# Kernel tuning notes

Measured on AMD Instinct MI355X. Metric: run time of the kernel, lower is better.

The kernel has to match this reference:

```python
import jax, jax.numpy as jnp
import numpy as np

H, D, HID = 16, 128, 2048
B, S = 2, 2048
NUM_BLOCKS, BLOCK_SIZE = 32, 128


def _rope(x, cos, sin):
    # x: [T, H, D]; cos/sin: [T, D/2] (neox / rotate-half style)
    half = x.shape[-1] // 2
    x1, x2 = x[..., :half], x[..., half:]
    c = cos[:, None, :]
    s = sin[:, None, :]
    return jnp.concatenate([x1 * c - x2 * s, x2 * c + x1 * s], axis=-1)


def setup_inputs() -> dict:
    key = jax.random.key(0)
    ks = jax.random.split(key, 6)
    T = B * S
    hidden_states = jax.random.normal(ks[0], (T, HID), jnp.float32)
    wqkv = jax.random.normal(ks[1], (HID, 3 * HID), jnp.float32) * 0.02
    bqkv = jax.random.normal(ks[2], (3 * HID,), jnp.float32) * 0.02
    wo = jax.random.normal(ks[3], (HID, HID), jnp.float32) * 0.02
    # rotary tables, base 10000, dim = head_size
    inv_freq = 1.0 / (10000.0 ** (jnp.arange(0, D, 2, dtype=jnp.float32) / D))  # [D/2]
    pos = jnp.tile(jnp.arange(S, dtype=jnp.float32), B)  # positions per token [T]
    ang = pos[:, None] * inv_freq[None, :]  # [T, D/2]
    cos, sin = jnp.cos(ang), jnp.sin(ang)
    k_cache = jnp.zeros((NUM_BLOCKS, BLOCK_SIZE, H, D), jnp.float32)
    v_cache = jnp.zeros((NUM_BLOCKS, BLOCK_SIZE, H, D), jnp.float32)
    cu_seqlen_prefill = jnp.array([0, S, 2 * S], jnp.int32)
    slots = jnp.arange(T, dtype=jnp.int32)
    return {"hidden_states": hidden_states, "cos": cos, "sin": sin,
            "wqkv": wqkv, "bqkv": bqkv, "wo": wo,
            "k_cache": k_cache, "v_cache": v_cache,
            "cu_seqlen_prefill": cu_seqlen_prefill, "slots": slots, "max_s": S}


def reference(hidden_states, cos, sin, wqkv, bqkv, wo, k_cache, v_cache,
              cu_seqlen_prefill, slots, max_s):
    T = hidden_states.shape[0]
    # fused QKV projection (c_attn)
    qkv = hidden_states @ wqkv + bqkv  # [T, 3*H*D]
    q, k, v = jnp.split(qkv, [H * D, 2 * H * D], axis=1)
    q = q.reshape(T, H, D)
    k = k.reshape(T, H, D)
    v = v.reshape(T, H, D)
    # rotary embedding on q and k (in-place in torch; functional here)
    q = _rope(q, cos, sin)
    k = _rope(k, cos, sin)
    # reshape_and_cache: scatter post-rope k and v into paged KV cache by slot
    kc = k_cache.reshape(-1, H, D).at[slots].set(k).reshape(k_cache.shape)
    vc = v_cache.reshape(-1, H, D).at[slots].set(v).reshape(v_cache.shape)
    # prefill flash attention: varlen causal; equal-length sequences here
    b, s = T // max_s, max_s
    qb = q.reshape(b, s, H, D)
    kb = k.reshape(b, s, H, D)
    vb = v.reshape(b, s, H, D)
    scale = D ** -0.5
    scores = jnp.einsum('bqhd,bkhd->bhqk', qb, kb) * scale  # [B,H,S,S]
    causal = jnp.tril(jnp.ones((s, s), bool))
    scores = jnp.where(causal[None, None], scores, jnp.finfo(scores.dtype).min)
    probs = jax.nn.softmax(scores, axis=-1)
    attn = jnp.einsum('bhqk,bkhd->bqhd', probs, vb).reshape(T, H * D)
    out = attn @ wo  # c_proj, no bias
    return out, kc, vc
```

## Files before the change

### kernel.cpp

```cpp
#include <hip/hip_runtime.h>

using f32x4  = __attribute__((ext_vector_type(4))) float;
using frag16 = __attribute__((ext_vector_type(8))) short;
using s16x4  = __attribute__((ext_vector_type(4))) short;
using s16x8  = __attribute__((ext_vector_type(8))) short;

#define DI __device__ __forceinline__

constexpr int HID  = 2048;
constexpr int NH   = 16;
constexpr int HD   = 128;
constexpr int TT   = 4096;
constexpr int SEQ  = 2048;
constexpr int NQKV = 3 * HID;

DI short f2bf(float f) {
  unsigned u = __builtin_bit_cast(unsigned, f);
  unsigned r = (u + 0x7fffu + ((u >> 16) & 1u)) >> 16;
  return (short)r;
}
DI float bf2f(short s) {
  unsigned u = ((unsigned)(unsigned short)s) << 16;
  return __builtin_bit_cast(float, u);
}

struct alignas(8) S4h { short a, b, c, d; };

__global__ void conv_f32_bf16(const float* __restrict__ in, short* __restrict__ out) {
  int gid = blockIdx.x * 256 + threadIdx.x;
  const float4* in4 = (const float4*)in;
  float4 v = in4[gid];
  S4h o{f2bf(v.x), f2bf(v.y), f2bf(v.z), f2bf(v.w)};
  ((S4h*)out)[gid] = o;
}

template <bool IN_F32>
__global__ void transpose_conv(const void* __restrict__ in_, short* __restrict__ out,
                               int ldin, int R) {
  __shared__ float t[64][65];
  const float* inf = (const float*)in_;
  const short* ins = (const short*)in_;
  int tid = threadIdx.x;
  int bx = blockIdx.x, by = blockIdx.y;
#pragma unroll
  for (int i = 0; i < 16; i++) {
    int idx = i * 256 + tid;
    int r = idx >> 6, c = idx & 63;
    size_t gi = (size_t)(by * 64 + r) * ldin + bx * 64 + c;
    t[r][c] = IN_F32 ? inf[gi] : bf2f(ins[gi]);
  }
  __syncthreads();
#pragma unroll
  for (int i = 0; i < 16; i++) {
    int idx = i * 256 + tid;
    int r = idx >> 6, c = idx & 63;
    out[(size_t)(bx * 64 + r) * R + by * 64 + c] = f2bf(t[c][r]);
  }
}

#define GLDS(src, dst)                                                     \
  __builtin_amdgcn_global_load_lds(                                        \
      (const __attribute__((address_space(1))) void*)(src),                \
      (__attribute__((address_space(3))) void*)(dst), 16, 0, 0)

template <bool ADD_BIAS, bool OUT_BF16>
__global__ __launch_bounds__(256, 2) void gemm_bt(
    const short* __restrict__ A, const short* __restrict__ Bt,
    const float* __restrict__ bias, void* __restrict__ Cout,
    int M, int N, int K) {
  __shared__ alignas(16) short Al[128 * 64];
  __shared__ alignas(16) short Bl[128 * 64];
  const int tid = threadIdx.x;
  const int wid = tid >> 6, lane = tid & 63;
  const int wr = wid >> 1, wc = wid & 1;
  const int l15 = lane & 15, lg = lane >> 4;
  const int row0 = blockIdx.y * 128, col0 = blockIdx.x * 128;
  const int lr8 = lane >> 3, l7 = lane & 7;

  f32x4 acc[4][4];
#pragma unroll
  for (int i = 0; i < 4; i++)
#pragma unroll
    for (int j = 0; j < 4; j++) acc[i][j] = {0.f, 0.f, 0.f, 0.f};

  for (int kt = 0; kt < K; kt += 64) {
#pragma unroll
    for (int c = 0; c < 4; c++) {
      int chunk = c * 4 + wid;
      int r = chunk * 8 + lr8;
      int ke = (l7 * 8) ^ ((r & 7) * 8);
      GLDS(A + (size_t)(row0 + r) * K + kt + ke, Al + chunk * 512);
      GLDS(Bt + (size_t)(col0 + r) * K + kt + ke, Bl + chunk * 512);
    }
    __syncthreads();
#pragma unroll
    for (int kk = 0; kk < 2; kk++) {
      frag16 af[4], bfv[4];
#pragma unroll
      for (int ai = 0; ai < 4; ai++) {
        int r = wr * 64 + ai * 16 + l15;
        int k0 = kk * 32 + lg * 8;
        af[ai] = *(const frag16*)(Al + r * 64 + (k0 ^ ((r & 7) * 8)));
      }
#pragma unroll
      for (int bj = 0; bj < 4; bj++) {
        int r = wc * 64 + bj * 16 + l15;
        int k0 = kk * 32 + lg * 8;
        bfv[bj] = *(const frag16*)(Bl + r * 64 + (k0 ^ ((r & 7) * 8)));
      }
#pragma unroll
      for (int ai = 0; ai < 4; ai++)
#pragma unroll
        for (int bj = 0; bj < 4; bj++)
          acc[ai][bj] = __builtin_amdgcn_mfma_f32_16x16x32_bf16(
              af[ai], bfv[bj], acc[ai][bj], 0, 0, 0);
    }
    __syncthreads();
  }
#pragma unroll
  for (int ai = 0; ai < 4; ai++) {
#pragma unroll
    for (int bj = 0; bj < 4; bj++) {
      int row = row0 + wr * 64 + ai * 16 + lg * 4;
      int col = col0 + wc * 64 + bj * 16 + l15;
      float bv = 0.f;
      if (ADD_BIAS) bv = bias[col];
#pragma unroll
      for (int r = 0; r < 4; r++) {
        float v = acc[ai][bj][r] + bv;
        if (OUT_BF16)
          ((short*)Cout)[(size_t)(row + r) * N + col] = f2bf(v);
        else
          ((float*)Cout)[(size_t)(row + r) * N + col] = v;
      }
    }
  }
}

__global__ void rope_scatter(const short* __restrict__ qkv, const float* __restrict__ cs,
                             const float* __restrict__ sn, const int* __restrict__ slots,
                             short* __restrict__ Qb, short* __restrict__ Kb,
                             float* __restrict__ kc, float* __restrict__ vc) {
  const int t = blockIdx.x;
  const int tid = threadIdx.x;
  const int slot = slots[t];
  const short* row = qkv + (size_t)t * NQKV;
  short* qo = Qb + (size_t)t * HID;
  short* ko = Kb + (size_t)t * HID;
  float* kco = kc + (size_t)slot * HID;
  float* vco = vc + (size_t)slot * HID;

  const int h = tid >> 4, d0 = (tid & 15) * 4;
  const int c1 = h * 128 + d0, c2 = c1 + 64;
  float4 c4 = *(const float4*)(cs + (size_t)t * 64 + d0);
  float4 s4 = *(const float4*)(sn + (size_t)t * 64 + d0);
  float cc[4] = {c4.x, c4.y, c4.z, c4.w};
  float ssv[4] = {s4.x, s4.y, s4.z, s4.w};
  s16x4 q1 = *(const s16x4*)(row + c1);
  s16x4 q2 = *(const s16x4*)(row + c2);
  s16x4 k1 = *(const s16x4*)(row + HID + c1);
  s16x4 k2 = *(const s16x4*)(row + HID + c2);
  s16x4 qo1, qo2, ko1, ko2;
  float kcv1[4], kcv2[4];
#pragma unroll
  for (int r = 0; r < 4; r++) {
    float a = bf2f(q1[r]), b = bf2f(q2[r]);
    qo1[r] = f2bf(a * cc[r] - b * ssv[r]);
    qo2[r] = f2bf(b * cc[r] + a * ssv[r]);
    float ka = bf2f(k1[r]), kb = bf2f(k2[r]);
    float o1 = ka * cc[r] - kb * ssv[r];
    float o2 = kb * cc[r] + ka * ssv[r];
    ko1[r] = f2bf(o1);
    ko2[r] = f2bf(o2);
    kcv1[r] = o1;
    kcv2[r] = o2;
  }
  *(s16x4*)(qo + c1) = qo1;
  *(s16x4*)(qo + c2) = qo2;
  *(s16x4*)(ko + c1) = ko1;
  *(s16x4*)(ko + c2) = ko2;
  *(float4*)(kco + c1) = {kcv1[0], kcv1[1], kcv1[2], kcv1[3]};
  *(float4*)(kco + c2) = {kcv2[0], kcv2[1], kcv2[2], kcv2[3]};

  const int vi = tid * 8;
  s16x8 v8 = *(const s16x8*)(row + 2 * HID + vi);
  *(float4*)(vco + vi)     = {bf2f(v8[0]), bf2f(v8[1]), bf2f(v8[2]), bf2f(v8[3])};
  *(float4*)(vco + vi + 4) = {bf2f(v8[4]), bf2f(v8[5]), bf2f(v8[6]), bf2f(v8[7])};
}

__global__ __launch_bounds__(256, 2) void flash_attn3(
    const short* __restrict__ Qb, const short* __restrict__ Kb,
    const short* __restrict__ Vt, short* __restrict__ attn) {
  __shared__ alignas(16) short Klds[2][32 * 128];
  __shared__ alignas(16) short Vlds[2][128 * 32];
  __shared__ alignas(16) short plds[4][16 * 40];

  const int tid = threadIdx.x;
  const int w = tid >> 6, lane = tid & 63;
  const int l15 = lane & 15, lg = lane >> 4;
  const int bid = blockIdx.x;
  const int pr = bid >> 5;
  const int bh = bid & 31;
  const int b = bh >> 4, h = bh & 15;
  short* pl = &plds[w][0];
  const float scale = 0.08838834764831845f;

  frag16 ones;
#pragma unroll
  for (int j = 0; j < 8; j++) ones[j] = (short)0x3F80;

  auto stage = [&](int kv0, int buf) {
#pragma unroll
    for (int ci = 0; ci < 2; ci++) {
      int e = ci * 256 + w * 64 + lane;
      int row = e >> 4, sp = e & 15;
      int ss = sp ^ (row & 15);
      GLDS(Kb + (size_t)(b * SEQ + kv0 + row) * HID + h * HD + ss * 8,
           &Klds[buf][(ci * 256 + w * 64) * 8]);
    }
#pragma unroll
    for (int ci = 0; ci < 2; ci++) {
      int e = ci * 256 + w * 64 + lane;
      int d = e >> 2, sp = e & 3;
      int ss = sp ^ (d & 3);
      GLDS(Vt + (size_t)(h * HD + d) * TT + b * SEQ + kv0 + ss * 8,
           &Vlds[buf][(ci * 256 + w * 64) * 8]);
    }
  };

  const int strips[2] = {31 - pr, pr};
#pragma unroll 1
  for (int spi = 0; spi < 2; spi++) {
    const int s = strips[spi];
    const int qrow0 = s * 64 + w * 16;
    const int nt = 2 * s + 2;

    frag16 qf[4];
    {
      const short* qp = Qb + (size_t)(b * SEQ + qrow0 + l15) * HID + h * HD + lg * 8;
#pragma unroll
      for (int ds = 0; ds < 4; ds++) qf[ds] = *(const frag16*)(qp + ds * 32);
    }
    f32x4 o[8];
#pragma unroll
    for (int j = 0; j < 8; j++) o[j] = {0.f, 0.f, 0.f, 0.f};
    f32x4 la = {0.f, 0.f, 0.f, 0.f};
    float mr[4] = {-1e30f, -1e30f, -1e30f, -1e30f};

    stage(0, 0);
    __syncthreads();

    int cur = 0;
    for (int t = 0; t < nt; t++) {
      const int kv0 = t * 32;
      if (t + 1 < nt) stage(kv0 + 32, cur ^ 1);

      if (kv0 <= qrow0 + 15) {
        const short* Kl = &Klds[cur][0];
        const short* Vl = &Vlds[cur][0];
        f32x4 sa0 = {0.f, 0.f, 0.f, 0.f}, sa1 = {0.f, 0.f, 0.f, 0.f};
#pragma unroll
        for (int ds = 0; ds < 4; ds++) {
          int phys = (ds * 4 + lg) ^ l15;
          frag16 kf0 = *(const frag16*)(Kl + l15 * 128 + phys * 8);
          frag16 kf1 = *(const frag16*)(Kl + (16 + l15) * 128 + phys * 8);
          sa0 = __builtin_amdgcn_mfma_f32_16x16x32_bf16(qf[ds], kf0, sa0, 0, 0, 0);
          sa1 = __builtin_amdgcn_mfma_f32_16x16x32_bf16(qf[ds], kf1, sa1, 0, 0, 0);
        }
        float s0[4], s1[4], pm[4];
        const bool mk = (kv0 + 31 > qrow0);
#pragma unroll
        for (int r = 0; r < 4; r++) {
          s0[r] = sa0[r] * scale;
          s1[r] = sa1[r] * scale;
          if (mk) {
            int qi = qrow0 + lg * 4 + r;
            if (kv0 + l15 > qi) s0[r] = -1e30f;
            if (kv0 + 16 + l15 > qi) s1[r] = -1e30f;
          }
          pm[r] = fmaxf(s0[r], s1[r]);
        }
#pragma unroll
        for (int m = 1; m < 16; m <<= 1)
#pragma unroll
          for (int r = 0; r < 4; r++) pm[r] = fmaxf(pm[r], __shfl_xor(pm[r], m));
        bool need = false;
#pragma unroll
        for (int r = 0; r < 4; r++) need = need || (pm[r] > mr[r] + 8.f);
        if (__any(need)) {
#pragma unroll
          for (int r = 0; r < 4; r++) {
            float mn = fmaxf(mr[r], pm[r]);
            float fr = __expf(mr[r] - mn);
            mr[r] = mn;
            la[r] *= fr;
#pragma unroll
            for (int j = 0; j < 8; j++) o[j][r] *= fr;
          }
        }
#pragma unroll
        for (int r = 0; r < 4; r++) {
          float p0 = __expf(s0[r] - mr[r]);
          float p1 = __expf(s1[r] - mr[r]);
          pl[(lg * 4 + r) * 40 + l15] = f2bf(p0);
          pl[(lg * 4 + r) * 40 + 16 + l15] = f2bf(p1);
        }
        asm volatile("s_waitcnt lgkmcnt(0)" ::: "memory");
        frag16 pf = *(const frag16*)(pl + l15 * 40 + lg * 8);
        la = __builtin_amdgcn_mfma_f32_16x16x32_bf16(pf, ones, la, 0, 0, 0);
#pragma unroll
        for (int j = 0; j < 8; j++) {
          int d = j * 16 + l15;
          int phys = lg ^ (d & 3);
          frag16 vf = *(const frag16*)(Vl + d * 32 + phys * 8);
          o[j] = __builtin_amdgcn_mfma_f32_16x16x32_bf16(pf, vf, o[j], 0, 0, 0);
        }
      }
      __syncthreads();
      cur ^= 1;
    }

    float inv[4];
#pragma unroll
    for (int r = 0; r < 4; r++) inv[r] = 1.f / la[r];
    short* op = attn + (size_t)(b * SEQ + qrow0 + lg * 4) * HID + h * HD + l15;
#pragma unroll
    for (int j = 0; j < 8; j++)
#pragma unroll
      for (int r = 0; r < 4; r++)
        op[(size_t)r * HID + j * 16] = f2bf(o[j][r] * inv[r]);
    __syncthreads();
  }
}

extern "C" void kernel_launch(void* const* d_in, const int* in_sizes, int n_in,
                              void* d_out, int out_size, void* d_ws, size_t ws_size,
                              hipStream_t stream) {
  const float* hidden = (const float*)d_in[0];
  const float* cosb   = (const float*)d_in[1];
  const float* sinb   = (const float*)d_in[2];
  const float* wqkv   = (const float*)d_in[3];
  const float* bqkv   = (const float*)d_in[4];
  const float* wo     = (const float*)d_in[5];
  const int*   slots  = (const int*)d_in[9];

  float* out = (float*)d_out;
  float* kc  = out + (size_t)TT * HID;
  float* vc  = kc + (size_t)TT * HID;

  short* ws    = (short*)d_ws;
  short* Abf   = ws;
  short* Wqkvt = Abf + 8388608;
  short* Wot   = Wqkvt + 12582912;
  short* qkvb  = Wot + 4194304;
  short* Qb    = qkvb + 25165824;
  short* Kb    = Qb + 8388608;
  short* Vt    = Kb + 8388608;
  short* attnb = Abf;

  conv_f32_bf16<<<8192, 256, 0, stream>>>(hidden, Abf);
  transpose_conv<true><<<dim3(96, 32), 256, 0, stream>>>(wqkv, Wqkvt, NQKV, HID);
  transpose_conv<true><<<dim3(32, 32), 256, 0, stream>>>(wo, Wot, HID, HID);
  gemm_bt<true, true><<<dim3(48, 32), 256, 0, stream>>>(Abf, Wqkvt, bqkv, qkvb,
                                                        TT, NQKV, HID);
  rope_scatter<<<TT, 256, 0, stream>>>(qkvb, cosb, sinb, slots, Qb, Kb, kc, vc);
  transpose_conv<false><<<dim3(32, 64), 256, 0, stream>>>(qkvb + 2 * HID, Vt, NQKV, TT);
  flash_attn3<<<512, 256, 0, stream>>>(Qb, Kb, Vt, attnb);
  gemm_bt<false, false><<<dim3(16, 32), 256, 0, stream>>>(attnb, Wot, nullptr, out,
                                                          TT, HID, HID);
}
```

Baseline: 319.4 us.

## Rework flash attention to 64-key tiles with transposed S and exp2 scaling

The flash attention kernel now processes 64 keys per tile instead of 32 and computes S transposed (K as the A operand), so each lane holds one query's scores and row max reduction needs only two shuffles. The softmax scale times log2(e) is folded into Q inside the rope kernel, which allows exp2f with no per-element scale multiply. P is packed to bf16 with v_cvt_pk_bf16_f32, and V is written with a permuted key order so its layout matches the new P fragment layout. The GEMM also gets an XCD-style block-index swizzle, and a redundant syncthreads is dropped; the larger LDS tiles may lower occupancy.

```diff
diff --git a/kernel.cpp b/kernel.cpp
--- a/kernel.cpp
+++ b/kernel.cpp
@@ -4,6 +4,7 @@
 using frag16 = __attribute__((ext_vector_type(8))) short;
 using s16x4  = __attribute__((ext_vector_type(4))) short;
 using s16x8  = __attribute__((ext_vector_type(8))) short;
+using u32x4  = __attribute__((ext_vector_type(4))) unsigned;
 
 #define DI __device__ __forceinline__
 
@@ -23,6 +24,11 @@
   unsigned u = ((unsigned)(unsigned short)s) << 16;
   return __builtin_bit_cast(float, u);
 }
+DI unsigned cvtpk(float lo, float hi) {
+  unsigned r;
+  asm("v_cvt_pk_bf16_f32 %0, %1, %2" : "=v"(r) : "v"(lo), "v"(hi));
+  return r;
+}
 
 struct alignas(8) S4h { short a, b, c, d; };
 
@@ -34,7 +40,7 @@
   ((S4h*)out)[gid] = o;
 }
 
-template <bool IN_F32>
+template <bool IN_F32, bool PERM>
 __global__ void transpose_conv(const void* __restrict__ in_, short* __restrict__ out,
                                int ldin, int R) {
   __shared__ float t[64][65];
@@ -54,7 +60,8 @@
   for (int i = 0; i < 16; i++) {
     int idx = i * 256 + tid;
     int r = idx >> 6, c = idx & 63;
-    out[(size_t)(bx * 64 + r) * R + by * 64 + c] = f2bf(t[c][r]);
+    int cs = PERM ? (16 * (c & 3) + 4 * (c >> 4) + ((c >> 2) & 3)) : c;
+    out[(size_t)(bx * 64 + r) * R + by * 64 + c] = f2bf(t[cs][r]);
   }
 }
 
@@ -74,7 +81,11 @@
   const int wid = tid >> 6, lane = tid & 63;
   const int wr = wid >> 1, wc = wid & 1;
   const int l15 = lane & 15, lg = lane >> 4;
-  const int row0 = blockIdx.y * 128, col0 = blockIdx.x * 128;
+  const int gx = gridDim.x;
+  const int id = blockIdx.y * gx + blockIdx.x;
+  const int nwg = gx * gridDim.y;
+  const int swz = (id & 7) * (nwg >> 3) + (id >> 3);
+  const int row0 = (swz / gx) * 128, col0 = (swz % gx) * 128;
   const int lr8 = lane >> 3, l7 = lane & 7;
 
   f32x4 acc[4][4];
@@ -141,6 +152,7 @@
                              const float* __restrict__ sn, const int* __restrict__ slots,
                              short* __restrict__ Qb, short* __restrict__ Kb,
                              float* __restrict__ kc, float* __restrict__ vc) {
+  const float SCL = 0.08838834764831845f * 1.4426950408889634f;
   const int t = blockIdx.x;
   const int tid = threadIdx.x;
   const int slot = slots[t];
@@ -165,8 +177,8 @@
 #pragma unroll
   for (int r = 0; r < 4; r++) {
     float a = bf2f(q1[r]), b = bf2f(q2[r]);
-    qo1[r] = f2bf(a * cc[r] - b * ssv[r]);
-    qo2[r] = f2bf(b * cc[r] + a * ssv[r]);
+    qo1[r] = f2bf((a * cc[r] - b * ssv[r]) * SCL);
+    qo2[r] = f2bf((b * cc[r] + a * ssv[r]) * SCL);
     float ka = bf2f(k1[r]), kb = bf2f(k2[r]);
     float o1 = ka * cc[r] - kb * ssv[r];
     float o2 = kb * cc[r] + ka * ssv[r];
@@ -188,12 +200,12 @@
   *(float4*)(vco + vi + 4) = {bf2f(v8[4]), bf2f(v8[5]), bf2f(v8[6]), bf2f(v8[7])};
 }
 
-__global__ __launch_bounds__(256, 2) void flash_attn3(
+__global__ __launch_bounds__(256, 2) void flash_attn4(
     const short* __restrict__ Qb, const short* __restrict__ Kb,
     const short* __restrict__ Vt, short* __restrict__ attn) {
-  __shared__ alignas(16) short Klds[2][32 * 128];
-  __shared__ alignas(16) short Vlds[2][128 * 32];
-  __shared__ alignas(16) short plds[4][16 * 40];
+  __shared__ alignas(16) short Klds[2][64 * 128];
+  __shared__ alignas(16) short Vlds[2][128 * 64];
+  __shared__ alignas(16) short plds[4][16 * 72];
 
   const int tid = threadIdx.x;
   const int w = tid >> 6, lane = tid & 63;
@@ -203,7 +215,6 @@
   const int bh = bid & 31;
   const int b = bh >> 4, h = bh & 15;
   short* pl = &plds[w][0];
-  const float scale = 0.08838834764831845f;
 
   frag16 ones;
 #pragma unroll
@@ -211,20 +222,18 @@
 
   auto stage = [&](int kv0, int buf) {
 #pragma unroll
-    for (int ci = 0; ci < 2; ci++) {
-      int e = ci * 256 + w * 64 + lane;
-      int row = e >> 4, sp = e & 15;
-      int ss = sp ^ (row & 15);
-      GLDS(Kb + (size_t)(b * SEQ + kv0 + row) * HID + h * HD + ss * 8,
-           &Klds[buf][(ci * 256 + w * 64) * 8]);
-    }
-#pragma unroll
-    for (int ci = 0; ci < 2; ci++) {
-      int e = ci * 256 + w * 64 + lane;
-      int d = e >> 2, sp = e & 3;
-      int ss = sp ^ (d & 3);
-      GLDS(Vt + (size_t)(h * HD + d) * TT + b * SEQ + kv0 + ss * 8,
-           &Vlds[buf][(ci * 256 + w * 64) * 8]);
+    for (int ci = 0; ci < 4; ci++) {
+      int cc = w * 4 + ci;
+      int krow = cc * 4 + (lane >> 4);
+      int ksp = lane & 15;
+      int kss = ksp ^ (krow & 15);
+      GLDS(Kb + (size_t)(b * SEQ + kv0 + krow) * HID + h * HD + kss * 8,
+           Klds[buf] + cc * 512);
+      int vd = cc * 8 + (lane >> 3);
+      int vsp = lane & 7;
+      int vss = vsp ^ (vd & 7);
+      GLDS(Vt + (size_t)(h * HD + vd) * TT + b * SEQ + kv0 + vss * 8,
+           Vlds[buf] + cc * 512);
     }
   };
 
@@ -233,7 +242,7 @@
   for (int spi = 0; spi < 2; spi++) {
     const int s = strips[spi];
     const int qrow0 = s * 64 + w * 16;
-    const int nt = 2 * s + 2;
+    const int nt = s + 1;
 
     frag16 qf[4];
     {
@@ -245,76 +254,90 @@
 #pragma unroll
     for (int j = 0; j < 8; j++) o[j] = {0.f, 0.f, 0.f, 0.f};
     f32x4 la = {0.f, 0.f, 0.f, 0.f};
-    float mr[4] = {-1e30f, -1e30f, -1e30f, -1e30f};
+    float mr = -1e30f;
 
     stage(0, 0);
     __syncthreads();
 
     int cur = 0;
     for (int t = 0; t < nt; t++) {
-      const int kv0 = t * 32;
-      if (t + 1 < nt) stage(kv0 + 32, cur ^ 1);
-
-      if (kv0 <= qrow0 + 15) {
-        const short* Kl = &Klds[cur][0];
-        const short* Vl = &Vlds[cur][0];
-        f32x4 sa0 = {0.f, 0.f, 0.f, 0.f}, sa1 = {0.f, 0.f, 0.f, 0.f};
-#pragma unroll
-        for (int ds = 0; ds < 4; ds++) {
-          int phys = (ds * 4 + lg) ^ l15;
-          frag16 kf0 = *(const frag16*)(Kl + l15 * 128 + phys * 8);
-          frag16 kf1 = *(const frag16*)(Kl + (16 + l15) * 128 + phys * 8);
-          sa0 = __builtin_amdgcn_mfma_f32_16x16x32_bf16(qf[ds], kf0, sa0, 0, 0, 0);
-          sa1 = __builtin_amdgcn_mfma_f32_16x16x32_bf16(qf[ds], kf1, sa1, 0, 0, 0);
+      const int kv0 = t * 64;
+      if (t + 1 < nt) stage(kv0 + 64, cur ^ 1);
+
+      const short* Kl = &Klds[cur][0];
+      const short* Vl = &Vlds[cur][0];
+      f32x4 sa[4];
+#pragma unroll
+      for (int f = 0; f < 4; f++) sa[f] = {0.f, 0.f, 0.f, 0.f};
+#pragma unroll
+      for (int ds = 0; ds < 4; ds++) {
+        int phys = (ds * 4 + lg) ^ l15;
+#pragma unroll
+        for (int f = 0; f < 4; f++) {
+          frag16 kf = *(const frag16*)(Kl + (f * 16 + l15) * 128 + phys * 8);
+          sa[f] = __builtin_amdgcn_mfma_f32_16x16x32_bf16(kf, qf[ds], sa[f], 0, 0, 0);
         }
-        float s0[4], s1[4], pm[4];
-        const bool mk = (kv0 + 31 > qrow0);
+      }
+      if (kv0 + 63 > qrow0) {
+        int ql = 16 * w + l15;
+#pragma unroll
+        for (int f = 0; f < 4; f++)
+#pragma unroll
+          for (int r = 0; r < 4; r++)
+            if (f * 16 + lg * 4 + r > ql) sa[f][r] = -1e30f;
+      }
+      float pm = sa[0][0];
+#pragma unroll
+      for (int f = 0; f < 4; f++)
+#pragma unroll
+        for (int r = 0; r < 4; r++) pm = fmaxf(pm, sa[f][r]);
+      pm = fmaxf(pm, __shfl_xor(pm, 16));
+      pm = fmaxf(pm, __shfl_xor(pm, 32));
+      if (__any(pm > mr + 8.f)) {
+        float mn = fmaxf(mr, pm);
+        float frl = exp2f(mr - mn);
+        mr = mn;
+        float fr4[4];
+#pragma unroll
+        for (int r = 0; r < 4; r++)
+          fr4[r] = __shfl(frl, lg * 16 + lg * 4 + r);
 #pragma unroll
         for (int r = 0; r < 4; r++) {
-          s0[r] = sa0[r] * scale;
-          s1[r] = sa1[r] * scale;
-          if (mk) {
-            int qi = qrow0 + lg * 4 + r;
-            if (kv0 + l15 > qi) s0[r] = -1e30f;
-            if (kv0 + 16 + l15 > qi) s1[r] = -1e30f;
-          }
-          pm[r] = fmaxf(s0[r], s1[r]);
+          la[r] *= fr4[r];
+#pragma unroll
+          for (int j = 0; j < 8; j++) o[j][r] *= fr4[r];
         }
-#pragma unroll
-        for (int m = 1; m < 16; m <<= 1)
-#pragma unroll
-          for (int r = 0; r < 4; r++) pm[r] = fmaxf(pm[r], __shfl_xor(pm[r], m));
-        bool need = false;
-#pragma unroll
-        for (int r = 0; r < 4; r++) need = need || (pm[r] > mr[r] + 8.f);
-        if (__any(need)) {
-#pragma unroll
-          for (int r = 0; r < 4; r++) {
-            float mn = fmaxf(mr[r], pm[r]);
-            float fr = __expf(mr[r] - mn);
-            mr[r] = mn;
-            la[r] *= fr;
-#pragma unroll
-            for (int j = 0; j < 8; j++) o[j][r] *= fr;
-          }
-        }
-#pragma unroll
-        for (int r = 0; r < 4; r++) {
-          float p0 = __expf(s0[r] - mr[r]);
-          float p1 = __expf(s1[r] - mr[r]);
-          pl[(lg * 4 + r) * 40 + l15] = f2bf(p0);
-          pl[(lg * 4 + r) * 40 + 16 + l15] = f2bf(p1);
-        }
-        asm volatile("s_waitcnt lgkmcnt(0)" ::: "memory");
-        frag16 pf = *(const frag16*)(pl + l15 * 40 + lg * 8);
-        la = __builtin_amdgcn_mfma_f32_16x16x32_bf16(pf, ones, la, 0, 0, 0);
-#pragma unroll
-        for (int j = 0; j < 8; j++) {
-          int d = j * 16 + l15;
-          int phys = lg ^ (d & 3);
-          frag16 vf = *(const frag16*)(Vl + d * 32 + phys * 8);
-          o[j] = __builtin_amdgcn_mfma_f32_16x16x32_bf16(pf, vf, o[j], 0, 0, 0);
-        }
+      }
+      float pe[4][4];
+#pragma unroll
+      for (int f = 0; f < 4; f++)
+#pragma unroll
+        for (int r = 0; r < 4; r++) pe[f][r] = exp2f(sa[f][r] - mr);
+      unsigned wv[8];
+#pragma unroll
+      for (int r = 0; r < 4; r++) {
+        wv[2 * r]     = cvtpk(pe[0][r], pe[1][r]);
+        wv[2 * r + 1] = cvtpk(pe[2][r], pe[3][r]);
+      }
+      {
+        u32x4* pb = (u32x4*)(pl + l15 * 72 + lg * 16);
+        pb[0] = {wv[0], wv[1], wv[2], wv[3]};
+        pb[1] = {wv[4], wv[5], wv[6], wv[7]};
+      }
+      asm volatile("s_waitcnt lgkmcnt(0)" ::: "memory");
+      frag16 pf0 = *(const frag16*)(pl + l15 * 72 + lg * 8);
+      frag16 pf1 = *(const frag16*)(pl + l15 * 72 + 32 + lg * 8);
+      la = __builtin_amdgcn_mfma_f32_16x16x32_bf16(pf0, ones, la, 0, 0, 0);
+      la = __builtin_amdgcn_mfma_f32_16x16x32_bf16(pf1, ones, la, 0, 0, 0);
+#pragma unroll
+      for (int j = 0; j < 8; j++) {
+        int d = j * 16 + l15;
+        int p0 = lg ^ (d & 7);
+        int p1 = (4 + lg) ^ (d & 7);
+        frag16 vf0 = *(const frag16*)(Vl + d * 64 + p0 * 8);
+        frag16 vf1 = *(const frag16*)(Vl + d * 64 + p1 * 8);
+        o[j] = __builtin_amdgcn_mfma_f32_16x16x32_bf16(pf0, vf0, o[j], 0, 0, 0);
+        o[j] = __builtin_amdgcn_mfma_f32_16x16x32_bf16(pf1, vf1, o[j], 0, 0, 0);
       }
       __syncthreads();
       cur ^= 1;
@@ -329,7 +352,6 @@
 #pragma unroll
       for (int r = 0; r < 4; r++)
         op[(size_t)r * HID + j * 16] = f2bf(o[j][r] * inv[r]);
-    __syncthreads();
   }
 }
 
@@ -359,13 +381,13 @@
   short* attnb = Abf;
 
   conv_f32_bf16<<<8192, 256, 0, stream>>>(hidden, Abf);
-  transpose_conv<true><<<dim3(96, 32), 256, 0, stream>>>(wqkv, Wqkvt, NQKV, HID);
-  transpose_conv<true><<<dim3(32, 32), 256, 0, stream>>>(wo, Wot, HID, HID);
+  transpose_conv<true, false><<<dim3(96, 32), 256, 0, stream>>>(wqkv, Wqkvt, NQKV, HID);
+  transpose_conv<true, false><<<dim3(32, 32), 256, 0, stream>>>(wo, Wot, HID, HID);
   gemm_bt<true, true><<<dim3(48, 32), 256, 0, stream>>>(Abf, Wqkvt, bqkv, qkvb,
                                                         TT, NQKV, HID);
   rope_scatter<<<TT, 256, 0, stream>>>(qkvb, cosb, sinb, slots, Qb, Kb, kc, vc);
-  transpose_conv<false><<<dim3(32, 64), 256, 0, stream>>>(qkvb + 2 * HID, Vt, NQKV, TT);
-  flash_attn3<<<512, 256, 0, stream>>>(Qb, Kb, Vt, attnb);
+  transpose_conv<false, true><<<dim3(32, 64), 256, 0, stream>>>(qkvb + 2 * HID, Vt, NQKV, TT);
+  flash_attn4<<<512, 256, 0, stream>>>(Qb, Kb, Vt, attnb);
   gemm_bt<false, false><<<dim3(16, 32), 256, 0, stream>>>(attnb, Wot, nullptr, out,
                                                           TT, HID, HID);
 }
```

Result: faster. 297.9 us (-6.7%).
